# Performance work log

Hardware: AMD Instinct MI355X
Metric: run time of the kernel (lower is better)

Reference implementation:

```python
import jax, jax.numpy as jnp
import numpy as np

N, CM, CZ, COPM = 256, 384, 128, 32
HS, DHS = 8, 48   # row-attention heads / head dim (HS*DHS == CM)
HT, DHT = 4, 32   # triangle-attention heads / head dim


def _param_shapes():
    d = {'opm_ln': (2, CM), 'opm_lr_w': (2, CM, COPM), 'opm_lr_b': (2, COPM),
         'opm_out_w': (COPM, COPM, CZ), 'opm_out_b': (CZ,),
         'ra_ln': (2, CM), 'ra_pair_ln': (2, CZ), 'ra_feat_w': (CZ, HS),
         'ra_qkv_w': (3, CM, HS, DHS), 'ra_gate_w': (CM, HS, DHS), 'ra_gate_b': (HS, DHS),
         'ra_o_w': (HS, DHS, CM), 'ra_o_b': (CM,),
         'st_ln': (2, CM), 'st_w1': (CM, 4 * CM), 'st_b1': (4 * CM,), 'st_w2': (4 * CM, CM), 'st_b2': (CM,)}
    for p in ('tmo', 'tmi'):
        d.update({p + '_ln': (2, CZ), p + '_lr_w': (2, CZ, CZ), p + '_lr_b': (2, CZ),
                  p + '_gate_w': (2, CZ, CZ), p + '_gate_b': (2, CZ), p + '_cln': (2, CZ),
                  p + '_out_w': (CZ, CZ), p + '_out_b': (CZ,), p + '_og_w': (CZ, CZ), p + '_og_b': (CZ,)})
    for p in ('tas', 'tae'):
        d.update({p + '_ln': (2, CZ), p + '_feat_w': (CZ, HT), p + '_qkv_w': (3, CZ, HT, DHT),
                  p + '_gate_w': (CZ, HT, DHT), p + '_gate_b': (HT, DHT),
                  p + '_o_w': (HT, DHT, CZ), p + '_o_b': (CZ,)})
    d.update({'pt_ln': (2, CZ), 'pt_w1': (CZ, 4 * CZ), 'pt_b1': (4 * CZ,),
              'pt_w2': (4 * CZ, CZ), 'pt_b2': (CZ,)})
    return d

_PNAMES = list(_param_shapes().keys())


def setup_inputs():
    keys = iter(jax.random.split(jax.random.key(0), 64))
    inp = {'single_act': jax.random.normal(next(keys), (1, N, CM), jnp.float32),
           'pair_act': jax.random.normal(next(keys), (N, N, CZ), jnp.float32),
           'single_mask': jnp.ones((1, N), jnp.float32),
           'pair_mask': jnp.ones((N, N), jnp.float32)}
    for name, shp in _param_shapes().items():
        p = 0.1 * jax.random.normal(next(keys), shp, jnp.float32)
        if name.endswith('_ln') or name.endswith('_cln'):
            p = p.at[0].add(1.0)  # LayerNorm scale centered at 1
        inp[name] = p
    return inp


def _ln(x, p, eps=1e-5):
    mu = jnp.mean(x, -1, keepdims=True)
    var = jnp.var(x, -1, keepdims=True)
    return (x - mu) * jax.lax.rsqrt(var + eps) * p[0] + p[1]


def _attn(q_data, m_data, bias, nb, qkv_w, gw, gb, ow, ob):
    # AlphaFold gated attention with nonbatched pair bias.
    dh = qkv_w.shape[-1]
    q = jnp.einsum('bqa,ahc->bqhc', q_data, qkv_w[0]) * (dh ** -0.5)
    k = jnp.einsum('bka,ahc->bkhc', m_data, qkv_w[1])
    v = jnp.einsum('bka,ahc->bkhc', m_data, qkv_w[2])
    logits = jnp.einsum('bqhc,bkhc->bhqk', q, k) + bias + nb[None]
    w = jax.nn.softmax(logits, axis=-1)
    wa = jnp.einsum('bhqk,bkhc->bqhc', w, v)
    wa = wa * jax.nn.sigmoid(jnp.einsum('bqc,chv->bqhv', q_data, gw) + gb)
    return jnp.einsum('bqhc,hco->bqo', wa, ow) + ob


def _opm(single, mask1, ln_p, lr_w, lr_b, out_w, out_b):
    # Outer-stack(product)-mean: single [S=1,N,CM] -> pair update [N,N,CZ]
    x = _ln(single, ln_p)
    m = mask1[..., None]
    left = m * (x @ lr_w[0] + lr_b[0])    # [1,N,COPM]
    right = m * (x @ lr_w[1] + lr_b[1])
    act = jnp.einsum('abc,ade->dceb', left, right)          # [N,COPM,COPM,N]
    act = jnp.einsum('dceb,cef->dbf', act, out_w) + out_b   # [N,N,CZ]
    norm = jnp.einsum('abc,adc->bdc', m, m)                 # [N,N,1]
    return act / (1e-3 + norm)


def _tri_mult(pair, mask2, ln_p, lr_w, lr_b, gw, gb, cln, out_w, out_b, og_w, og_b, outgoing):
    m = mask2[..., None]
    x = _ln(pair, ln_p)
    left = m * (x @ lr_w[0] + lr_b[0]) * jax.nn.sigmoid(x @ gw[0] + gb[0])
    right = m * (x @ lr_w[1] + lr_b[1]) * jax.nn.sigmoid(x @ gw[1] + gb[1])
    eq = 'ikc,jkc->ijc' if outgoing else 'kjc,kic->ijc'
    out = jnp.einsum(eq, left, right)
    out = _ln(out, cln) @ out_w + out_b
    out = out * jax.nn.sigmoid(x @ og_w + og_b)
    return pair + out


def _tri_attn(pair, mask2, ln_p, feat_w, qkv_w, gw, gb, ow, ob, per_column):
    pa = jnp.swapaxes(pair, 0, 1) if per_column else pair
    mk = jnp.swapaxes(mask2, 0, 1) if per_column else mask2
    x = _ln(pa, ln_p)
    bias = (1e9 * (mk - 1.0))[:, None, None, :]
    nb = jnp.einsum('qkc,ch->hqk', x, feat_w)
    out = _attn(x, x, bias, nb, qkv_w, gw, gb, ow, ob)
    if per_column:
        out = jnp.swapaxes(out, 0, 1)
    return pair + out


def _fwd(sa, pa, sm, pm, p):
    # 1) outer stack mean -> pair residual
    pa = pa + _opm(sa, sm, p['opm_ln'], p['opm_lr_w'], p['opm_lr_b'], p['opm_out_w'], p['opm_out_b'])
    # 2) row attention with pair bias
    x = _ln(sa, p['ra_ln'])
    bias = (1e9 * (sm - 1.0))[:, None, None, :]
    nb = jnp.einsum('qkc,ch->hqk', _ln(pa, p['ra_pair_ln']), p['ra_feat_w'])
    sa = sa + _attn(x, x, bias, nb, p['ra_qkv_w'], p['ra_gate_w'], p['ra_gate_b'], p['ra_o_w'], p['ra_o_b'])
    # 3) single transition
    x = _ln(sa, p['st_ln'])
    sa = sa + jax.nn.relu(x @ p['st_w1'] + p['st_b1']) @ p['st_w2'] + p['st_b2']
    # 4/5) triangle multiplications
    ko = ('ln', 'lr_w', 'lr_b', 'gate_w', 'gate_b', 'cln', 'out_w', 'out_b', 'og_w', 'og_b')
    pa = _tri_mult(pa, pm, *[p['tmo_' + k] for k in ko], outgoing=True)
    pa = _tri_mult(pa, pm, *[p['tmi_' + k] for k in ko], outgoing=False)
    # 6/7) triangle attentions
    ka = ('ln', 'feat_w', 'qkv_w', 'gate_w', 'gate_b', 'o_w', 'o_b')
    pa = _tri_attn(pa, pm, *[p['tas_' + k] for k in ka], per_column=False)
    pa = _tri_attn(pa, pm, *[p['tae_' + k] for k in ka], per_column=True)
    # 8) pair transition
    x = _ln(pa, p['pt_ln'])
    pa = pa + jax.nn.relu(x @ p['pt_w1'] + p['pt_b1']) @ p['pt_w2'] + p['pt_b2']
    return sa, pa


def reference(single_act, pair_act, single_mask, pair_mask,
              opm_ln, opm_lr_w, opm_lr_b, opm_out_w, opm_out_b,
              ra_ln, ra_pair_ln, ra_feat_w, ra_qkv_w, ra_gate_w, ra_gate_b, ra_o_w, ra_o_b,
              st_ln, st_w1, st_b1, st_w2, st_b2,
              tmo_ln, tmo_lr_w, tmo_lr_b, tmo_gate_w, tmo_gate_b, tmo_cln, tmo_out_w, tmo_out_b, tmo_og_w, tmo_og_b,
              tmi_ln, tmi_lr_w, tmi_lr_b, tmi_gate_w, tmi_gate_b, tmi_cln, tmi_out_w, tmi_out_b, tmi_og_w, tmi_og_b,
              tas_ln, tas_feat_w, tas_qkv_w, tas_gate_w, tas_gate_b, tas_o_w, tas_o_b,
              tae_ln, tae_feat_w, tae_qkv_w, tae_gate_w, tae_gate_b, tae_o_w, tae_o_b,
              pt_ln, pt_w1, pt_b1, pt_w2, pt_b2):
    args = dict(locals())
    p = {k: args[k] for k in _PNAMES}
    return _fwd(single_act, pair_act, single_mask, pair_mask, p)
```

## Files before the change

### kernel.cpp

```cpp
#include <hip/hip_runtime.h>
#include <math.h>

typedef long long i64;
#define NN_ 65536L

typedef __attribute__((ext_vector_type(8))) short bf16x8;
typedef __attribute__((ext_vector_type(4))) float f32x4;

__device__ inline unsigned short f2bf(float f){
  unsigned int u = __float_as_uint(f);
  return (unsigned short)((u + 0x7FFFu + ((u>>16)&1u)) >> 16);
}

__global__ __launch_bounds__(256) void copy_k(float* __restrict__ d, const float* __restrict__ s, long n){
  long i = (long)blockIdx.x*blockDim.x + threadIdx.x;
  if (i < n) d[i] = s[i];
}

__global__ __launch_bounds__(256) void chw2hwc_k(const float* __restrict__ in, float* __restrict__ out){
  __shared__ float t[32][33];
  int r0 = blockIdx.x*32, c0 = blockIdx.y*32;
  int tx = threadIdx.x & 31, ty = threadIdx.x >> 5;
  for (int i = ty; i < 32; i += 8) t[i][tx] = in[(i64)(c0+i)*NN_ + r0 + tx];
  __syncthreads();
  for (int i = ty; i < 32; i += 8) out[(i64)(r0+i)*128 + c0 + tx] = t[tx][i];
}

__global__ __launch_bounds__(256) void tr_mask_k(const float* __restrict__ in, const float* __restrict__ mask,
                                                 float* __restrict__ out){
  __shared__ float t[32][33];
  int r0 = blockIdx.x*32, c0 = blockIdx.y*32;
  int tx = threadIdx.x & 31, ty = threadIdx.x >> 5;
  for (int i = ty; i < 32; i += 8) t[i][tx] = in[(i64)(r0+i)*128 + c0 + tx];
  __syncthreads();
  for (int i = ty; i < 32; i += 8) out[(i64)(c0+i)*NN_ + r0 + tx] = t[tx][i] * mask[r0+tx];
}

__global__ __launch_bounds__(256) void feat4_k(const float* __restrict__ X, const float* __restrict__ W,
                                               float* __restrict__ out){
  __shared__ float4 w_s[128];
  int q = blockIdx.x, k = threadIdx.x;
  if (k < 128) w_s[k] = *(const float4*)(W + k*4);
  __syncthreads();
  const float* x = X + ((i64)q*256 + k)*128;
  float a0=0.f, a1=0.f, a2=0.f, a3=0.f;
  #pragma unroll
  for (int c=0;c<128;c+=4){
    float4 v = *(const float4*)(x+c);
    float4 w0 = w_s[c], w1 = w_s[c+1], w2 = w_s[c+2], w3 = w_s[c+3];
    a0 = fmaf(v.x,w0.x,a0); a1 = fmaf(v.x,w0.y,a1); a2 = fmaf(v.x,w0.z,a2); a3 = fmaf(v.x,w0.w,a3);
    a0 = fmaf(v.y,w1.x,a0); a1 = fmaf(v.y,w1.y,a1); a2 = fmaf(v.y,w1.z,a2); a3 = fmaf(v.y,w1.w,a3);
    a0 = fmaf(v.z,w2.x,a0); a1 = fmaf(v.z,w2.y,a1); a2 = fmaf(v.z,w2.z,a2); a3 = fmaf(v.z,w2.w,a3);
    a0 = fmaf(v.w,w3.x,a0); a1 = fmaf(v.w,w3.y,a1); a2 = fmaf(v.w,w3.z,a2); a3 = fmaf(v.w,w3.w,a3);
  }
  i64 o = (i64)q*256 + k;
  out[o] = a0; out[65536+o] = a1; out[131072+o] = a2; out[196608+o] = a3;
}

__global__ __launch_bounds__(256) void feat8_k(const float* __restrict__ X, const float* __restrict__ W,
                                               float* __restrict__ out){
  __shared__ float w_s[128][8];
  int q = blockIdx.x, k = threadIdx.x;
  for (int i = k; i < 1024; i += 256) ((float*)w_s)[i] = W[i];
  __syncthreads();
  const float* x = X + ((i64)q*256 + k)*128;
  float acc[8] = {};
  #pragma unroll
  for (int c=0;c<128;c+=4){
    float4 v = *(const float4*)(x+c);
    #pragma unroll
    for (int h=0;h<8;h++){
      acc[h] = fmaf(v.x, w_s[c  ][h], acc[h]);
      acc[h] = fmaf(v.y, w_s[c+1][h], acc[h]);
      acc[h] = fmaf(v.z, w_s[c+2][h], acc[h]);
      acc[h] = fmaf(v.w, w_s[c+3][h], acc[h]);
    }
  }
  float* o = out + ((i64)q*256 + k)*8;
  *(float4*)o     = make_float4(acc[0],acc[1],acc[2],acc[3]);
  *(float4*)(o+4) = make_float4(acc[4],acc[5],acc[6],acc[7]);
}

__global__ __launch_bounds__(128) void ln_k(const float* __restrict__ in, float* __restrict__ out,
                                            const float* __restrict__ w, int C){
  i64 row = blockIdx.x;
  const float* x = in + row*C;
  float* y = out + row*C;
  int tid = threadIdx.x;
  float s=0.f, s2=0.f;
  for (int c=tid;c<C;c+=128){ float v = x[c]; s += v; s2 += v*v; }
  __shared__ float rs[128], rq[128];
  rs[tid]=s; rq[tid]=s2; __syncthreads();
  for (int off=64;off>0;off>>=1){ if (tid<off){ rs[tid]+=rs[tid+off]; rq[tid]+=rq[tid+off]; } __syncthreads(); }
  float mu = rs[0]/C;
  float var = rq[0]/C - mu*mu;
  float inv = rsqrtf(var + 1e-5f);
  for (int c=tid;c<C;c+=128) y[c] = (x[c]-mu)*inv*w[c] + w[C+c];
}

__global__ __launch_bounds__(256) void ln128_k(const float* __restrict__ in, float* __restrict__ out,
                                               const float* __restrict__ w, int T){
  int wv = threadIdx.x >> 6, lane = threadIdx.x & 63;
  i64 row = (i64)blockIdx.x*4 + wv;
  i64 rr = T ? (i64)((((int)row & 255) << 8) | ((int)row >> 8)) : row;
  float2 v = *(const float2*)(in + rr*128 + lane*2);
  float s = v.x + v.y, s2 = v.x*v.x + v.y*v.y;
  #pragma unroll
  for (int off=32; off; off>>=1){ s += __shfl_down(s, off); s2 += __shfl_down(s2, off); }
  s = __shfl(s, 0); s2 = __shfl(s2, 0);
  float mu = s*(1.f/128.f);
  float var = s2*(1.f/128.f) - mu*mu;
  float inv = rsqrtf(var + 1e-5f);
  float2 wl = *(const float2*)(w + lane*2);
  float2 wb = *(const float2*)(w + 128 + lane*2);
  float2 y; y.x = (v.x-mu)*inv*wl.x + wb.x; y.y = (v.y-mu)*inv*wl.y + wb.y;
  *(float2*)(out + row*128 + lane*2) = y;
}

template<bool TA, bool TB>
__global__ __launch_bounds__(256) void mgemm_k(
    const float* __restrict__ A, int lda, i64 sA,
    const float* __restrict__ B, int ldb, i64 sB,
    float* __restrict__ C, int ldc, i64 sC,
    int M, int N, int K,
    const float* __restrict__ bias, float scale, int act,
    const float* __restrict__ rowmul, int combine, const float* __restrict__ aux)
{
  A += (i64)blockIdx.z * sA;
  B += (i64)blockIdx.z * sB;
  C += (i64)blockIdx.z * sC;
  int m0 = blockIdx.x * 128, n0 = blockIdx.y * 128;
  int tid = threadIdx.x;
  int wave = tid >> 6, lane = tid & 63;
  int quad = lane >> 4, mr = lane & 15;
  int wm = (wave >> 1) * 64, wn = (wave & 1) * 64;
  __shared__ unsigned short As[128][40];
  __shared__ unsigned short Bs[128][40];
  f32x4 acc[4][4];
  #pragma unroll
  for (int i=0;i<4;i++)
    #pragma unroll
    for (int j=0;j<4;j++) acc[i][j] = (f32x4){0.f,0.f,0.f,0.f};

  for (int k0 = 0; k0 < K; k0 += 32){
    if (!TA){
      #pragma unroll
      for (int it=0; it<4; it++){
        int lin = tid + it*256;
        int r = lin >> 3, c4 = (lin & 7) * 4;
        float4 g = *(const float4*)&A[(i64)(m0+r)*lda + k0 + c4];
        As[r][c4]   = f2bf(g.x); As[r][c4+1] = f2bf(g.y);
        As[r][c4+2] = f2bf(g.z); As[r][c4+3] = f2bf(g.w);
      }
    } else {
      #pragma unroll
      for (int it=0; it<4; it++){
        int lin = tid + it*256;
        int m = lin & 127, kg = (lin >> 7) * 4;
        float v0 = A[(i64)(k0+kg  )*lda + m0 + m];
        float v1 = A[(i64)(k0+kg+1)*lda + m0 + m];
        float v2 = A[(i64)(k0+kg+2)*lda + m0 + m];
        float v3 = A[(i64)(k0+kg+3)*lda + m0 + m];
        As[m][kg] = f2bf(v0); As[m][kg+1] = f2bf(v1);
        As[m][kg+2] = f2bf(v2); As[m][kg+3] = f2bf(v3);
      }
    }
    if (!TB){
      #pragma unroll
      for (int it=0; it<4; it++){
        int lin = tid + it*256;
        int n = lin & 127, kg = (lin >> 7) * 4;
        float v0 = B[(i64)(k0+kg  )*ldb + n0 + n];
        float v1 = B[(i64)(k0+kg+1)*ldb + n0 + n];
        float v2 = B[(i64)(k0+kg+2)*ldb + n0 + n];
        float v3 = B[(i64)(k0+kg+3)*ldb + n0 + n];
        Bs[n][kg] = f2bf(v0); Bs[n][kg+1] = f2bf(v1);
        Bs[n][kg+2] = f2bf(v2); Bs[n][kg+3] = f2bf(v3);
      }
    } else {
      #pragma unroll
      for (int it=0; it<4; it++){
        int lin = tid + it*256;
        int r = lin >> 3, c4 = (lin & 7) * 4;
        float4 g = *(const float4*)&B[(i64)(n0+r)*ldb + k0 + c4];
        Bs[r][c4]   = f2bf(g.x); Bs[r][c4+1] = f2bf(g.y);
        Bs[r][c4+2] = f2bf(g.z); Bs[r][c4+3] = f2bf(g.w);
      }
    }
    __syncthreads();
    bf16x8 af[4], bfr[4];
    #pragma unroll
    for (int i=0;i<4;i++) af[i]  = *(const bf16x8*)&As[wm + i*16 + mr][quad*8];
    #pragma unroll
    for (int j=0;j<4;j++) bfr[j] = *(const bf16x8*)&Bs[wn + j*16 + mr][quad*8];
    #pragma unroll
    for (int i=0;i<4;i++)
      #pragma unroll
      for (int j=0;j<4;j++)
        acc[i][j] = __builtin_amdgcn_mfma_f32_16x16x32_bf16(af[i], bfr[j], acc[i][j], 0, 0, 0);
    __syncthreads();
  }
  #pragma unroll
  for (int i=0;i<4;i++){
    #pragma unroll
    for (int r=0;r<4;r++){
      int m = m0 + wm + i*16 + quad*4 + r;
      float rm = rowmul ? rowmul[m] : 1.f;
      i64 mrow = (combine == 4) ? (i64)(((m & 255) << 8) | (m >> 8)) : (i64)m;
      #pragma unroll
      for (int j=0;j<4;j++){
        int n = n0 + wn + j*16 + mr;
        float v = acc[i][j][r] * scale;
        if (bias) v += bias[n];
        if (act == 1) v = fmaxf(v, 0.f);
        else if (act == 2) v = 1.f/(1.f + __expf(-v));
        v *= rm;
        i64 idx = mrow*ldc + n;
        if (combine == 0) C[idx] = v;
        else if (combine == 1 || combine == 4) C[idx] += v;
        else if (combine == 2) C[idx] *= v;
        else C[idx] += aux[(i64)m*ldc + n] * v;
      }
    }
  }
}

template<bool TA, bool TB>
__global__ __launch_bounds__(256) void mgemm64_k(
    const float* __restrict__ A, int lda, i64 sA,
    const float* __restrict__ B, int ldb, i64 sB,
    float* __restrict__ C, int ldc, i64 sC,
    int M, int N, int K,
    const float* __restrict__ bias, float scale, int act,
    const float* __restrict__ rowmul, int combine, const float* __restrict__ aux)
{
  A += (i64)blockIdx.z * sA;
  B += (i64)blockIdx.z * sB;
  C += (i64)blockIdx.z * sC;
  int m0 = blockIdx.x * 64, n0 = blockIdx.y * 64;
  int tid = threadIdx.x;
  int wave = tid >> 6, lane = tid & 63;
  int quad = lane >> 4, mr = lane & 15;
  int wm = (wave >> 1) * 32, wn = (wave & 1) * 32;
  __shared__ unsigned short As[64][40];
  __shared__ unsigned short Bs[64][40];
  f32x4 acc[2][2];
  #pragma unroll
  for (int i=0;i<2;i++)
    #pragma unroll
    for (int j=0;j<2;j++) acc[i][j] = (f32x4){0.f,0.f,0.f,0.f};

  for (int k0 = 0; k0 < K; k0 += 32){
    if (!TA){
      #pragma unroll
      for (int it=0; it<2; it++){
        int lin = tid + it*256;
        int r = lin >> 3, c4 = (lin & 7) * 4;
        float4 g = *(const float4*)&A[(i64)(m0+r)*lda + k0 + c4];
        As[r][c4]   = f2bf(g.x); As[r][c4+1] = f2bf(g.y);
        As[r][c4+2] = f2bf(g.z); As[r][c4+3] = f2bf(g.w);
      }
    } else {
      #pragma unroll
      for (int it=0; it<2; it++){
        int lin = tid + it*256;
        int m = lin & 63, kg = (lin >> 6) * 4;
        float v0 = A[(i64)(k0+kg  )*lda + m0 + m];
        float v1 = A[(i64)(k0+kg+1)*lda + m0 + m];
        float v2 = A[(i64)(k0+kg+2)*lda + m0 + m];
        float v3 = A[(i64)(k0+kg+3)*lda + m0 + m];
        As[m][kg] = f2bf(v0); As[m][kg+1] = f2bf(v1);
        As[m][kg+2] = f2bf(v2); As[m][kg+3] = f2bf(v3);
      }
    }
    if (!TB){
      #pragma unroll
      for (int it=0; it<2; it++){
        int lin = tid + it*256;
        int n = lin & 63, kg = (lin >> 6) * 4;
        float v0 = B[(i64)(k0+kg  )*ldb + n0 + n];
        float v1 = B[(i64)(k0+kg+1)*ldb + n0 + n];
        float v2 = B[(i64)(k0+kg+2)*ldb + n0 + n];
        float v3 = B[(i64)(k0+kg+3)*ldb + n0 + n];
        Bs[n][kg] = f2bf(v0); Bs[n][kg+1] = f2bf(v1);
        Bs[n][kg+2] = f2bf(v2); Bs[n][kg+3] = f2bf(v3);
      }
    } else {
      #pragma unroll
      for (int it=0; it<2; it++){
        int lin = tid + it*256;
        int r = lin >> 3, c4 = (lin & 7) * 4;
        float4 g = *(const float4*)&B[(i64)(n0+r)*ldb + k0 + c4];
        Bs[r][c4]   = f2bf(g.x); Bs[r][c4+1] = f2bf(g.y);
        Bs[r][c4+2] = f2bf(g.z); Bs[r][c4+3] = f2bf(g.w);
      }
    }
    __syncthreads();
    bf16x8 af[2], bfr[2];
    #pragma unroll
    for (int i=0;i<2;i++) af[i]  = *(const bf16x8*)&As[wm + i*16 + mr][quad*8];
    #pragma unroll
    for (int j=0;j<2;j++) bfr[j] = *(const bf16x8*)&Bs[wn + j*16 + mr][quad*8];
    #pragma unroll
    for (int i=0;i<2;i++)
      #pragma unroll
      for (int j=0;j<2;j++)
        acc[i][j] = __builtin_amdgcn_mfma_f32_16x16x32_bf16(af[i], bfr[j], acc[i][j], 0, 0, 0);
    __syncthreads();
  }
  #pragma unroll
  for (int i=0;i<2;i++){
    #pragma unroll
    for (int r=0;r<4;r++){
      int m = m0 + wm + i*16 + quad*4 + r;
      float rm = rowmul ? rowmul[m] : 1.f;
      i64 mrow = (combine == 4) ? (i64)(((m & 255) << 8) | (m >> 8)) : (i64)m;
      #pragma unroll
      for (int j=0;j<2;j++){
        int n = n0 + wn + j*16 + mr;
        float v = acc[i][j][r] * scale;
        if (bias) v += bias[n];
        if (act == 1) v = fmaxf(v, 0.f);
        else if (act == 2) v = 1.f/(1.f + __expf(-v));
        v *= rm;
        i64 idx = mrow*ldc + n;
        if (combine == 0) C[idx] = v;
        else if (combine == 1 || combine == 4) C[idx] += v;
        else if (combine == 2) C[idx] *= v;
        else C[idx] += aux[(i64)m*ldc + n] * v;
      }
    }
  }
}

__global__ __launch_bounds__(256) void qkvb_k(
    const float* __restrict__ A, const float* __restrict__ B,
    unsigned short* __restrict__ C, float scale)
{
  int m0 = blockIdx.x * 64, n0 = blockIdx.y * 64;
  int tid = threadIdx.x;
  int wave = tid >> 6, lane = tid & 63;
  int quad = lane >> 4, mr = lane & 15;
  int wm = (wave >> 1) * 32, wn = (wave & 1) * 32;
  __shared__ unsigned short As[64][40];
  __shared__ unsigned short Bs[64][40];
  f32x4 acc[2][2];
  #pragma unroll
  for (int i=0;i<2;i++)
    #pragma unroll
    for (int j=0;j<2;j++) acc[i][j] = (f32x4){0.f,0.f,0.f,0.f};

  for (int k0 = 0; k0 < 128; k0 += 32){
    #pragma unroll
    for (int it=0; it<2; it++){
      int lin = tid + it*256;
      int r = lin >> 3, c4 = (lin & 7) * 4;
      float4 g = *(const float4*)&A[(i64)(m0+r)*128 + k0 + c4];
      As[r][c4]   = f2bf(g.x); As[r][c4+1] = f2bf(g.y);
      As[r][c4+2] = f2bf(g.z); As[r][c4+3] = f2bf(g.w);
    }
    #pragma unroll
    for (int it=0; it<2; it++){
      int lin = tid + it*256;
      int n = lin & 63, kg = (lin >> 6) * 4;
      float v0 = B[(i64)(k0+kg  )*128 + n0 + n];
      float v1 = B[(i64)(k0+kg+1)*128 + n0 + n];
      float v2 = B[(i64)(k0+kg+2)*128 + n0 + n];
      float v3 = B[(i64)(k0+kg+3)*128 + n0 + n];
      Bs[n][kg] = f2bf(v0); Bs[n][kg+1] = f2bf(v1);
      Bs[n][kg+2] = f2bf(v2); Bs[n][kg+3] = f2bf(v3);
    }
    __syncthreads();
    bf16x8 af[2], bfr[2];
    #pragma unroll
    for (int i=0;i<2;i++) af[i]  = *(const bf16x8*)&As[wm + i*16 + mr][quad*8];
    #pragma unroll
    for (int j=0;j<2;j++) bfr[j] = *(const bf16x8*)&Bs[wn + j*16 + mr][quad*8];
    #pragma unroll
    for (int i=0;i<2;i++)
      #pragma unroll
      for (int j=0;j<2;j++)
        acc[i][j] = __builtin_amdgcn_mfma_f32_16x16x32_bf16(af[i], bfr[j], acc[i][j], 0, 0, 0);
    __syncthreads();
  }
  #pragma unroll
  for (int i=0;i<2;i++){
    #pragma unroll
    for (int r=0;r<4;r++){
      int m = m0 + wm + i*16 + quad*4 + r;
      #pragma unroll
      for (int j=0;j<2;j++){
        int n = n0 + wn + j*16 + mr;
        C[(i64)m*128 + n] = f2bf(acc[i][j][r] * scale);
      }
    }
  }
}

__global__ __launch_bounds__(256) void mlrgate_k(
    const float* __restrict__ X,
    const float* __restrict__ Wl, const float* __restrict__ bl,
    const float* __restrict__ Wg, const float* __restrict__ bg,
    float* __restrict__ Out)
{
  int m0 = blockIdx.x * 64, n0 = blockIdx.y * 64;
  int tid = threadIdx.x;
  int wave = tid >> 6, lane = tid & 63;
  int quad = lane >> 4, mr = lane & 15;
  int wm = (wave >> 1) * 32, wn = (wave & 1) * 32;
  __shared__ unsigned short As[64][40], B1s[64][40], B2s[64][40];
  f32x4 acc1[2][2], acc2[2][2];
  #pragma unroll
  for (int i=0;i<2;i++)
    #pragma unroll
    for (int j=0;j<2;j++){ acc1[i][j] = (f32x4){0,0,0,0}; acc2[i][j] = (f32x4){0,0,0,0}; }

  for (int k0 = 0; k0 < 128; k0 += 32){
    #pragma unroll
    for (int it=0; it<2; it++){
      int lin = tid + it*256;
      int r = lin >> 3, c4 = (lin & 7) * 4;
      float4 g = *(const float4*)&X[(i64)(m0+r)*128 + k0 + c4];
      As[r][c4]   = f2bf(g.x); As[r][c4+1] = f2bf(g.y);
      As[r][c4+2] = f2bf(g.z); As[r][c4+3] = f2bf(g.w);
    }
    #pragma unroll
    for (int it=0; it<2; it++){
      int lin = tid + it*256;
      int n = lin & 63, kg = (lin >> 6) * 4;
      float a0 = Wl[(i64)(k0+kg  )*128 + n0 + n];
      float a1 = Wl[(i64)(k0+kg+1)*128 + n0 + n];
      float a2 = Wl[(i64)(k0+kg+2)*128 + n0 + n];
      float a3 = Wl[(i64)(k0+kg+3)*128 + n0 + n];
      B1s[n][kg] = f2bf(a0); B1s[n][kg+1] = f2bf(a1);
      B1s[n][kg+2] = f2bf(a2); B1s[n][kg+3] = f2bf(a3);
      float g0 = Wg[(i64)(k0+kg  )*128 + n0 + n];
      float g1 = Wg[(i64)(k0+kg+1)*128 + n0 + n];
      float g2 = Wg[(i64)(k0+kg+2)*128 + n0 + n];
      float g3 = Wg[(i64)(k0+kg+3)*128 + n0 + n];
      B2s[n][kg] = f2bf(g0); B2s[n][kg+1] = f2bf(g1);
      B2s[n][kg+2] = f2bf(g2); B2s[n][kg+3] = f2bf(g3);
    }
    __syncthreads();
    bf16x8 af[2], b1f[2], b2f[2];
    #pragma unroll
    for (int i=0;i<2;i++) af[i]  = *(const bf16x8*)&As[wm + i*16 + mr][quad*8];
    #pragma unroll
    for (int j=0;j<2;j++){
      b1f[j] = *(const bf16x8*)&B1s[wn + j*16 + mr][quad*8];
      b2f[j] = *(const bf16x8*)&B2s[wn + j*16 + mr][quad*8];
    }
    #pragma unroll
    for (int i=0;i<2;i++)
      #pragma unroll
      for (int j=0;j<2;j++){
        acc1[i][j] = __builtin_amdgcn_mfma_f32_16x16x32_bf16(af[i], b1f[j], acc1[i][j], 0, 0, 0);
        acc2[i][j] = __builtin_amdgcn_mfma_f32_16x16x32_bf16(af[i], b2f[j], acc2[i][j], 0, 0, 0);
      }
    __syncthreads();
  }
  #pragma unroll
  for (int i=0;i<2;i++){
    #pragma unroll
    for (int r=0;r<4;r++){
      int m = m0 + wm + i*16 + quad*4 + r;
      #pragma unroll
      for (int j=0;j<2;j++){
        int n = wn + j*16 + mr;
        float lv = acc1[i][j][r] + bl[n0 + n];
        float gv = acc2[i][j][r] + bg[n0 + n];
        Out[(i64)m*128 + n0 + n] = lv * (1.f/(1.f + __expf(-gv)));
      }
    }
  }
}

__global__ __launch_bounds__(256) void ptw1_k(
    const float* __restrict__ X, const float* __restrict__ W1,
    const float* __restrict__ b1, unsigned short* __restrict__ H)
{
  int m0 = blockIdx.x * 128, n0 = blockIdx.y * 128;
  int tid = threadIdx.x;
  int wave = tid >> 6, lane = tid & 63;
  int quad = lane >> 4, mr = lane & 15;
  int wm = (wave >> 1) * 64, wn = (wave & 1) * 64;
  __shared__ unsigned short As[128][40];
  __shared__ unsigned short Bs[128][40];
  f32x4 acc[4][4];
  #pragma unroll
  for (int i=0;i<4;i++)
    #pragma unroll
    for (int j=0;j<4;j++) acc[i][j] = (f32x4){0.f,0.f,0.f,0.f};

  for (int k0 = 0; k0 < 128; k0 += 32){
    #pragma unroll
    for (int it=0; it<4; it++){
      int lin = tid + it*256;
      int r = lin >> 3, c4 = (lin & 7) * 4;
      float4 g = *(const float4*)&X[(i64)(m0+r)*128 + k0 + c4];
      As[r][c4]   = f2bf(g.x); As[r][c4+1] = f2bf(g.y);
      As[r][c4+2] = f2bf(g.z); As[r][c4+3] = f2bf(g.w);
    }
    #pragma unroll
    for (int it=0; it<4; it++){
      int lin = tid + it*256;
      int n = lin & 127, kg = (lin >> 7) * 4;
      float v0 = W1[(i64)(k0+kg  )*512 + n0 + n];
      float v1 = W1[(i64)(k0+kg+1)*512 + n0 + n];
      float v2 = W1[(i64)(k0+kg+2)*512 + n0 + n];
      float v3 = W1[(i64)(k0+kg+3)*512 + n0 + n];
      Bs[n][kg] = f2bf(v0); Bs[n][kg+1] = f2bf(v1);
      Bs[n][kg+2] = f2bf(v2); Bs[n][kg+3] = f2bf(v3);
    }
    __syncthreads();
    bf16x8 af[4], bfr[4];
    #pragma unroll
    for (int i=0;i<4;i++) af[i]  = *(const bf16x8*)&As[wm + i*16 + mr][quad*8];
    #pragma unroll
    for (int j=0;j<4;j++) bfr[j] = *(const bf16x8*)&Bs[wn + j*16 + mr][quad*8];
    #pragma unroll
    for (int i=0;i<4;i++)
      #pragma unroll
      for (int j=0;j<4;j++)
        acc[i][j] = __builtin_amdgcn_mfma_f32_16x16x32_bf16(af[i], bfr[j], acc[i][j], 0, 0, 0);
    __syncthreads();
  }
  #pragma unroll
  for (int i=0;i<4;i++){
    #pragma unroll
    for (int r=0;r<4;r++){
      int m = m0 + wm + i*16 + quad*4 + r;
      #pragma unroll
      for (int j=0;j<4;j++){
        int n = n0 + wn + j*16 + mr;
        float v = fmaxf(acc[i][j][r] + b1[n], 0.f);
        H[(i64)m*512 + n] = f2bf(v);
      }
    }
  }
}

__global__ __launch_bounds__(256) void ptw2_k(
    const unsigned short* __restrict__ H, const float* __restrict__ W2,
    const float* __restrict__ b2, float* __restrict__ pa)
{
  int m0 = blockIdx.x * 64, n0 = blockIdx.y * 64;
  int tid = threadIdx.x;
  int wave = tid >> 6, lane = tid & 63;
  int quad = lane >> 4, mr = lane & 15;
  int wm = (wave >> 1) * 32, wn = (wave & 1) * 32;
  __shared__ unsigned short As[64][40];
  __shared__ unsigned short Bs[64][40];
  f32x4 acc[2][2];
  #pragma unroll
  for (int i=0;i<2;i++)
    #pragma unroll
    for (int j=0;j<2;j++) acc[i][j] = (f32x4){0.f,0.f,0.f,0.f};

  for (int k0 = 0; k0 < 512; k0 += 32){
    #pragma unroll
    for (int it=0; it<2; it++){
      int lin = tid + it*256;
      int r = lin >> 3, c4 = (lin & 7) * 4;
      *(uint2*)&As[r][c4] = *(const uint2*)&H[(i64)(m0+r)*512 + k0 + c4];
    }
    #pragma unroll
    for (int it=0; it<2; it++){
      int lin = tid + it*256;
      int n = lin & 63, kg = (lin >> 6) * 4;
      float v0 = W2[(i64)(k0+kg  )*128 + n0 + n];
      float v1 = W2[(i64)(k0+kg+1)*128 + n0 + n];
      float v2 = W2[(i64)(k0+kg+2)*128 + n0 + n];
      float v3 = W2[(i64)(k0+kg+3)*128 + n0 + n];
      Bs[n][kg] = f2bf(v0); Bs[n][kg+1] = f2bf(v1);
      Bs[n][kg+2] = f2bf(v2); Bs[n][kg+3] = f2bf(v3);
    }
    __syncthreads();
    bf16x8 af[2], bfr[2];
    #pragma unroll
    for (int i=0;i<2;i++) af[i]  = *(const bf16x8*)&As[wm + i*16 + mr][quad*8];
    #pragma unroll
    for (int j=0;j<2;j++) bfr[j] = *(const bf16x8*)&Bs[wn + j*16 + mr][quad*8];
    #pragma unroll
    for (int i=0;i<2;i++)
      #pragma unroll
      for (int j=0;j<2;j++)
        acc[i][j] = __builtin_amdgcn_mfma_f32_16x16x32_bf16(af[i], bfr[j], acc[i][j], 0, 0, 0);
    __syncthreads();
  }
  #pragma unroll
  for (int i=0;i<2;i++){
    #pragma unroll
    for (int r=0;r<4;r++){
      int m = m0 + wm + i*16 + quad*4 + r;
      #pragma unroll
      for (int j=0;j<2;j++){
        int n = n0 + wn + j*16 + mr;
        pa[(i64)m*128 + n] += acc[i][j][r] + b2[n];
      }
    }
  }
}

template<bool TA, bool TB>
__global__ __launch_bounds__(256) void gemm_k(
    const float* __restrict__ A, int lda, i64 sA,
    const float* __restrict__ B, int ldb, i64 sB,
    float* __restrict__ C, int ldc, i64 sC,
    int M, int N, int K,
    const float* __restrict__ bias, float scale, int act,
    const float* __restrict__ rowmul, int combine)
{
  A += (i64)blockIdx.z * sA;
  B += (i64)blockIdx.z * sB;
  C += (i64)blockIdx.z * sC;
  int m0 = blockIdx.x * 64, n0 = blockIdx.y * 64;
  int tid = threadIdx.x, tx = tid & 15, ty = tid >> 4;
  __shared__ float As[16][68], Bs[16][68];
  float acc[4][4] = {};
  for (int k0 = 0; k0 < K; k0 += 16){
    if (TA){
      for (int l = tid; l < 1024; l += 256){
        int kk = l >> 6, mi = l & 63; int m = m0 + mi;
        As[kk][mi] = (m < M) ? A[(i64)(k0+kk)*lda + m] : 0.f;
      }
    } else {
      for (int l = tid; l < 1024; l += 256){
        int mi = l >> 4, kk = l & 15; int m = m0 + mi;
        As[kk][mi] = (m < M) ? A[(i64)m*lda + k0 + kk] : 0.f;
      }
    }
    if (TB){
      for (int l = tid; l < 1024; l += 256){
        int ni = l >> 4, kk = l & 15; int n = n0 + ni;
        Bs[kk][ni] = (n < N) ? B[(i64)n*ldb + k0 + kk] : 0.f;
      }
    } else {
      for (int l = tid; l < 1024; l += 256){
        int kk = l >> 6, ni = l & 63; int n = n0 + ni;
        Bs[kk][ni] = (n < N) ? B[(i64)(k0+kk)*ldb + n] : 0.f;
      }
    }
    __syncthreads();
    #pragma unroll
    for (int kk = 0; kk < 16; ++kk){
      float4 av4 = *(const float4*)&As[kk][ty*4];
      float4 bv4 = *(const float4*)&Bs[kk][tx*4];
      float av[4] = {av4.x, av4.y, av4.z, av4.w};
      float bv[4] = {bv4.x, bv4.y, bv4.z, bv4.w};
      #pragma unroll
      for (int i=0;i<4;i++)
        #pragma unroll
        for (int j=0;j<4;j++) acc[i][j] = fmaf(av[i], bv[j], acc[i][j]);
    }
    __syncthreads();
  }
  #pragma unroll
  for (int i=0;i<4;i++){
    int m = m0 + ty*4 + i;
    if (m >= M) continue;
    float rm = rowmul ? rowmul[m] : 1.f;
    #pragma unroll
    for (int j=0;j<4;j++){
      int n = n0 + tx*4 + j;
      if (n >= N) continue;
      float v = acc[i][j] * scale;
      if (bias) v += bias[n];
      if (act == 1) v = fmaxf(v, 0.f);
      else if (act == 2) v = 1.f/(1.f + expf(-v));
      v *= rm;
      i64 idx = (i64)m*ldc + n;
      if (combine == 0) C[idx] = v;
      else if (combine == 1) C[idx] += v;
      else C[idx] *= v;
    }
  }
}

__global__ __launch_bounds__(256) void gemm_part_k(
    const float* __restrict__ A, int lda,
    const float* __restrict__ B, int ldb,
    float* __restrict__ Cp, int M, int N, int K, int chunk)
{
  int m0 = blockIdx.x*16, n0 = blockIdx.y*64, z = blockIdx.z;
  int kb = z*chunk, ke = min(K, kb+chunk);
  int tid = threadIdx.x;
  int mi = tid >> 4, ni4 = (tid & 15)*4;
  __shared__ float As[16][17], Bs[16][68];
  float acc[4] = {0.f,0.f,0.f,0.f};
  for (int k0 = kb; k0 < ke; k0 += 16){
    { int r = tid>>4, c = tid&15; int m = m0+r;
      As[c][r] = (m < M) ? A[(i64)m*lda + k0 + c] : 0.f; }
    for (int l = tid; l < 1024; l += 256){
      int kk = l>>6, nn = l&63; int n = n0+nn;
      Bs[kk][nn] = (n < N) ? B[(i64)(k0+kk)*ldb + n] : 0.f;
    }
    __syncthreads();
    #pragma unroll
    for (int kk=0;kk<16;kk++){
      float a = As[kk][mi];
      float4 b = *(const float4*)&Bs[kk][ni4];
      acc[0]=fmaf(a,b.x,acc[0]); acc[1]=fmaf(a,b.y,acc[1]);
      acc[2]=fmaf(a,b.z,acc[2]); acc[3]=fmaf(a,b.w,acc[3]);
    }
    __syncthreads();
  }
  int m = m0+mi, n = n0+ni4;
  if (m < M && n < N) *(float4*)&Cp[((i64)z*M + m)*N + n] = *(float4*)acc;
}

__global__ __launch_bounds__(256) void gemm_reduce_k(
    const float* __restrict__ Cp, float* __restrict__ C, int ldc,
    int M, int N, int S,
    const float* __restrict__ bias, float scale, int act,
    const float* __restrict__ rowmul, int combine)
{
  i64 idx = (i64)blockIdx.x*256 + threadIdx.x;
  if (idx >= (i64)M*N) return;
  int m = (int)(idx / N), n = (int)(idx % N);
  float s = 0.f;
  for (int z=0; z<S; z++) s += Cp[(i64)z*M*N + idx];
  float v = s*scale;
  if (bias) v += bias[n];
  if (act == 1) v = fmaxf(v, 0.f);
  else if (act == 2) v = 1.f/(1.f + expf(-v));
  if (rowmul) v *= rowmul[m];
  i64 o = (i64)m*ldc + n;
  if (combine == 0) C[o] = v;
  else if (combine == 1) C[o] += v;
  else C[o] *= v;
}

__global__ __launch_bounds__(128) void opm_wd_k(const float* __restrict__ right, const float* __restrict__ W,
                                                float* __restrict__ Wd){
  int d = blockIdx.x, c = blockIdx.y, f = threadIdx.x;
  float acc = 0.f;
  #pragma unroll
  for (int e=0;e<32;e++) acc = fmaf(right[d*32+e], W[((i64)c*32+e)*128 + f], acc);
  Wd[((i64)d*32+c)*128 + f] = acc;
}

__global__ __launch_bounds__(128) void opm_final_k(const float* __restrict__ left, const float* __restrict__ Wd,
                                                   const float* __restrict__ ob, const float* __restrict__ sm,
                                                   const float* __restrict__ pair_act, float* __restrict__ pa){
  int d = blockIdx.x, b0 = blockIdx.y*16, f = threadIdx.x;
  __shared__ float wd_s[32][128];
  __shared__ float l_s[16][32];
  for (int c=0;c<32;c++) wd_s[c][f] = Wd[((i64)d*32+c)*128 + f];
  for (int l = f; l < 512; l += 128){ int bi=l>>5, c=l&31; l_s[bi][c] = left[(b0+bi)*32 + c]; }
  __syncthreads();
  float md = sm[d], obf = ob[f];
  for (int bi=0;bi<16;bi++){
    float acc = 0.f;
    #pragma unroll
    for (int c=0;c<32;c++) acc = fmaf(l_s[bi][c], wd_s[c][f], acc);
    int b = b0+bi;
    i64 idx = ((i64)d*256 + b)*128 + f;
    pa[idx] = pair_act[idx] + (acc + obf) / (1e-3f + md*sm[b]);
  }
}

__global__ __launch_bounds__(256) void ra_attn_k(const float* __restrict__ q, const float* __restrict__ k,
                                                 const float* __restrict__ v, const float* __restrict__ nb,
                                                 const float* __restrict__ sm, float* __restrict__ wa){
  int qi = blockIdx.x, h = blockIdx.y, tid = threadIdx.x;
  __shared__ float qv[48];
  __shared__ float p[256];
  __shared__ float red[256];
  if (tid < 48) qv[tid] = q[(i64)qi*384 + h*48 + tid];
  __syncthreads();
  float acc = 0.f;
  const float* kr = k + (i64)tid*384 + h*48;
  #pragma unroll
  for (int c=0;c<48;c++) acc = fmaf(qv[c], kr[c], acc);
  acc += 1e9f*(sm[tid]-1.f) + nb[((i64)qi*256 + tid)*8 + h];
  red[tid] = acc; __syncthreads();
  for (int off=128;off>0;off>>=1){ if (tid<off) red[tid] = fmaxf(red[tid], red[tid+off]); __syncthreads(); }
  float mx = red[0]; __syncthreads();
  float e = expf(acc - mx);
  red[tid] = e; __syncthreads();
  for (int off=128;off>0;off>>=1){ if (tid<off) red[tid] += red[tid+off]; __syncthreads(); }
  p[tid] = e / red[0];
  __syncthreads();
  if (tid < 48){
    float a = 0.f;
    for (int kk=0;kk<256;kk++) a = fmaf(p[kk], v[(i64)kk*384 + h*48 + tid], a);
    wa[(i64)qi*384 + h*48 + tid] = a;
  }
}

__global__ __launch_bounds__(256, 6) void ta_mfma_k(
    const unsigned short* __restrict__ q, const unsigned short* __restrict__ k,
    const unsigned short* __restrict__ v,
    const float* __restrict__ nbQ, const float* __restrict__ mask, int maskT,
    float* __restrict__ wa)
{
  int d = blockIdx.x;
  int xcd = d & 7, y = d >> 3;
  int b = xcd*32 + (y >> 4);
  int w = y & 15;
  int qblk = w & 3, h = w >> 2;
  int tid = threadIdx.x;
  int wave = tid >> 6, lane = tid & 63;
  int quad = lane >> 4, mr = lane & 15;
  const i64 base = ((i64)b*256)*128 + h*32;

  __shared__ __align__(16) unsigned short Ks[128][40];
  __shared__ __align__(16) unsigned short Vt[32][136];
  __shared__ __align__(16) float mask_s[256];
  __shared__ __align__(16) unsigned short Pl[4][16][40];

  mask_s[tid] = 1e9f * ((maskT ? mask[(i64)tid*256 + b] : mask[(i64)b*256 + tid]) - 1.f);

  int q0w = qblk*64 + wave*16;
  int qg = q0w + mr;
  const float* nbq = nbQ + (i64)h*65536 + (i64)qg*256;

  bf16x8 qf = *(const bf16x8*)(q + base + (i64)qg*128 + quad*8);

  f32x4 o0 = (f32x4){0,0,0,0}, o1 = (f32x4){0,0,0,0};
  float mm = -1e30f, ll = 0.f;

  for (int half = 0; half < 2; half++){
    __syncthreads();
    #pragma unroll
    for (int it=0; it<4; it++){
      int idx = it*256 + tid;
      int kl = idx >> 3, c4 = (idx & 7)*4;
      i64 roff = base + (i64)(half*128 + kl)*128 + c4;
      *(uint2*)&Ks[kl][c4] = *(const uint2*)(k + roff);
      uint2 gv = *(const uint2*)(v + roff);
      const unsigned short* pv = (const unsigned short*)&gv;
      Vt[c4  ][kl] = pv[0];
      Vt[c4+1][kl] = pv[1];
      Vt[c4+2][kl] = pv[2];
      Vt[c4+3][kl] = pv[3];
    }
    __syncthreads();

    #pragma unroll
    for (int it=0; it<4; it++){
      int kc = it*32;
      int kg = half*128 + kc;
      bf16x8 kf0 = *(const bf16x8*)&Ks[kc + mr][quad*8];
      bf16x8 kf1 = *(const bf16x8*)&Ks[kc + 16 + mr][quad*8];
      f32x4 s0 = __builtin_amdgcn_mfma_f32_16x16x32_bf16(kf0, qf, (f32x4){0,0,0,0}, 0, 0, 0);
      f32x4 s1 = __builtin_amdgcn_mfma_f32_16x16x32_bf16(kf1, qf, (f32x4){0,0,0,0}, 0, 0, 0);
      float4 nb0 = *(const float4*)(nbq + kg + quad*4);
      float4 nb1 = *(const float4*)(nbq + kg + 16 + quad*4);
      float4 mk0 = *(const float4*)&mask_s[kg + quad*4];
      float4 mk1 = *(const float4*)&mask_s[kg + 16 + quad*4];
      s0[0] += nb0.x + mk0.x; s0[1] += nb0.y + mk0.y; s0[2] += nb0.z + mk0.z; s0[3] += nb0.w + mk0.w;
      s1[0] += nb1.x + mk1.x; s1[1] += nb1.y + mk1.y; s1[2] += nb1.z + mk1.z; s1[3] += nb1.w + mk1.w;

      float tm = fmaxf(fmaxf(fmaxf(s0[0],s0[1]), fmaxf(s0[2],s0[3])),
                       fmaxf(fmaxf(s1[0],s1[1]), fmaxf(s1[2],s1[3])));
      tm = fmaxf(tm, __shfl_xor(tm, 16));
      tm = fmaxf(tm, __shfl_xor(tm, 32));
      float nm = fmaxf(mm, tm);
      float alpha = __expf(mm - nm);
      mm = nm;
      float e00 = __expf(s0[0]-nm), e01 = __expf(s0[1]-nm);
      float e02 = __expf(s0[2]-nm), e03 = __expf(s0[3]-nm);
      float e10 = __expf(s1[0]-nm), e11 = __expf(s1[1]-nm);
      float e12 = __expf(s1[2]-nm), e13 = __expf(s1[3]-nm);
      float ps = ((e00+e01) + (e02+e03)) + ((e10+e11) + (e12+e13));
      ps += __shfl_xor(ps, 16);
      ps += __shfl_xor(ps, 32);
      ll = ll*alpha + ps;
      o0 *= alpha; o1 *= alpha;
      unsigned int p0 = (unsigned int)f2bf(e00) | ((unsigned int)f2bf(e01)<<16);
      unsigned int p1 = (unsigned int)f2bf(e02) | ((unsigned int)f2bf(e03)<<16);
      unsigned int p2 = (unsigned int)f2bf(e10) | ((unsigned int)f2bf(e11)<<16);
      unsigned int p3 = (unsigned int)f2bf(e12) | ((unsigned int)f2bf(e13)<<16);
      *(uint2*)&Pl[wave][mr][quad*4]      = make_uint2(p0, p1);
      *(uint2*)&Pl[wave][mr][16 + quad*4] = make_uint2(p2, p3);
      bf16x8 pf  = *(const bf16x8*)&Pl[wave][mr][quad*8];
      bf16x8 vf0 = *(const bf16x8*)&Vt[mr     ][kc + quad*8];
      bf16x8 vf1 = *(const bf16x8*)&Vt[16 + mr][kc + quad*8];
      o0 = __builtin_amdgcn_mfma_f32_16x16x32_bf16(vf0, pf, o0, 0, 0, 0);
      o1 = __builtin_amdgcn_mfma_f32_16x16x32_bf16(vf1, pf, o1, 0, 0, 0);
    }
  }

  float inv = 1.f/ll;
  float* wp = wa + base + (i64)qg*128;
  *(float4*)(wp + quad*4)      = make_float4(o0[0]*inv, o0[1]*inv, o0[2]*inv, o0[3]*inv);
  *(float4*)(wp + 16 + quad*4) = make_float4(o1[0]*inv, o1[1]*inv, o1[2]*inv, o1[3]*inv);
}

static void gemm(hipStream_t st, bool TA, bool TB,
                 const float* A, int lda, i64 sA,
                 const float* B, int ldb, i64 sB,
                 float* C, int ldc, i64 sC,
                 int M, int N, int K, int batch,
                 const float* bias, float scale, int act,
                 const float* rowmul, int combine)
{
  dim3 g((M+63)/64, (N+63)/64, batch), bl(256);
  if (!TA && !TB)      gemm_k<false,false><<<g,bl,0,st>>>(A,lda,sA,B,ldb,sB,C,ldc,sC,M,N,K,bias,scale,act,rowmul,combine);
  else if (!TA &&  TB) gemm_k<false,true ><<<g,bl,0,st>>>(A,lda,sA,B,ldb,sB,C,ldc,sC,M,N,K,bias,scale,act,rowmul,combine);
  else                 gemm_k<true ,false><<<g,bl,0,st>>>(A,lda,sA,B,ldb,sB,C,ldc,sC,M,N,K,bias,scale,act,rowmul,combine);
}

static void mgemm(hipStream_t st, bool TA, bool TB,
                  const float* A, int lda, i64 sA,
                  const float* B, int ldb, i64 sB,
                  float* C, int ldc, i64 sC,
                  int M, int N, int K, int batch,
                  const float* bias, float scale, int act,
                  const float* rowmul, int combine, const float* aux = nullptr)
{
  dim3 bl(256);
  i64 nb128 = (i64)(M/128)*(N/128)*batch;
  if (nb128 < 1024 && (M % 64) == 0 && (N % 64) == 0){
    dim3 g(M/64, N/64, batch);
    if (!TA && !TB)      mgemm64_k<false,false><<<g,bl,0,st>>>(A,lda,sA,B,ldb,sB,C,ldc,sC,M,N,K,bias,scale,act,rowmul,combine,aux);
    else if (!TA &&  TB) mgemm64_k<false,true ><<<g,bl,0,st>>>(A,lda,sA,B,ldb,sB,C,ldc,sC,M,N,K,bias,scale,act,rowmul,combine,aux);
    else                 mgemm64_k<true ,false><<<g,bl,0,st>>>(A,lda,sA,B,ldb,sB,C,ldc,sC,M,N,K,bias,scale,act,rowmul,combine,aux);
    return;
  }
  dim3 g(M/128, N/128, batch);
  if (!TA && !TB)      mgemm_k<false,false><<<g,bl,0,st>>>(A,lda,sA,B,ldb,sB,C,ldc,sC,M,N,K,bias,scale,act,rowmul,combine,aux);
  else if (!TA &&  TB) mgemm_k<false,true ><<<g,bl,0,st>>>(A,lda,sA,B,ldb,sB,C,ldc,sC,M,N,K,bias,scale,act,rowmul,combine,aux);
  else                 mgemm_k<true ,false><<<g,bl,0,st>>>(A,lda,sA,B,ldb,sB,C,ldc,sC,M,N,K,bias,scale,act,rowmul,combine,aux);
}

static void gemm_thin(hipStream_t st,
                      const float* A, int lda, const float* B, int ldb,
                      float* C, int ldc, int M, int N, int K,
                      const float* bias, float scale, int act,
                      const float* rowmul, int combine, float* part)
{
  const int S = 8;
  int chunk = ((K/S + 15)/16)*16; if (chunk < 16) chunk = 16;
  dim3 g((M+15)/16, (N+63)/64, S);
  gemm_part_k<<<g,256,0,st>>>(A,lda,B,ldb,part,M,N,K,chunk);
  i64 t = (i64)M*N;
  gemm_reduce_k<<<(int)((t+255)/256),256,0,st>>>(part,C,ldc,M,N,S,bias,scale,act,rowmul,combine);
}

extern "C" void kernel_launch(void* const* d_in, const int* in_sizes, int n_in,
                              void* d_out, int out_size, void* d_ws, size_t ws_size,
                              hipStream_t stream)
{
  const float* IN[64];
  for (int i=0;i<n_in && i<64;i++) IN[i] = (const float*)d_in[i];

  const float* single_act = IN[0];
  const float* pair_act   = IN[1];
  const float* sm         = IN[2];
  const float* pm         = IN[3];
  const float* opm_ln     = IN[4];
  const float* opm_lr_w   = IN[5];
  const float* opm_lr_b   = IN[6];
  const float* opm_out_w  = IN[7];
  const float* opm_out_b  = IN[8];
  const float* ra_ln      = IN[9];
  const float* ra_pair_ln = IN[10];
  const float* ra_feat_w  = IN[11];
  const float* ra_qkv_w   = IN[12];
  const float* ra_gate_w  = IN[13];
  const float* ra_gate_b  = IN[14];
  const float* ra_o_w     = IN[15];
  const float* ra_o_b     = IN[16];
  const float* st_ln      = IN[17];
  const float* st_w1      = IN[18];
  const float* st_b1      = IN[19];
  const float* st_w2      = IN[20];
  const float* st_b2      = IN[21];
  const float* pt_ln      = IN[56];
  const float* pt_w1      = IN[57];
  const float* pt_b1      = IN[58];
  const float* pt_w2      = IN[59];
  const float* pt_b2      = IN[60];

  float* sa = (float*)d_out;
  float* pa = (float*)d_out + 98304;

  float* W  = (float*)d_ws;
  float* B0 = W;
  float* B1 = W + 8388608L;
  float* B2 = W + 16777216L;
  float* B3 = W + 25165824L;
  float* SMA = W + 33554432L;
  float* xs   = SMA;
  float* qb   = SMA +  98304;
  float* kb   = SMA + 196608;
  float* vb   = SMA + 294912;
  float* wab  = SMA + 393216;
  float* hst  = SMA + 491520;
  float* nbra = SMA + 884736;
  float* lbuf = SMA + 1409024;
  float* rbuf = SMA + 1417216;
  float* Wd   = SMA + 1425408;

  unsigned short* qb16 = (unsigned short*)B2;
  unsigned short* kb16 = (unsigned short*)B2 + 8388608L;
  unsigned short* vb16 = (unsigned short*)B3;

  copy_k<<<384, 256, 0, stream>>>(sa, single_act, 98304L);

  ln_k<<<256,128,0,stream>>>(single_act, xs, opm_ln, 384);
  gemm_thin(stream, xs,384, opm_lr_w,32,       lbuf,32, 256,32,384, opm_lr_b,    1.f,0, sm,0, B1);
  gemm_thin(stream, xs,384, opm_lr_w+12288,32, rbuf,32, 256,32,384, opm_lr_b+32, 1.f,0, sm,0, B1);
  opm_wd_k<<<dim3(256,32),128,0,stream>>>(rbuf, opm_out_w, Wd);
  opm_final_k<<<dim3(256,16),128,0,stream>>>(lbuf, Wd, opm_out_b, sm, pair_act, pa);

  ln_k<<<256,128,0,stream>>>(sa, xs, ra_ln, 384);
  ln128_k<<<16384,256,0,stream>>>(pa, B0, ra_pair_ln, 0);
  feat8_k<<<256,256,0,stream>>>(B0, ra_feat_w, nbra);
  const float qs_ra = 0.14433756729740643f;
  gemm_thin(stream, xs,384, ra_qkv_w,384,        qb,384, 256,384,384, nullptr,qs_ra,0,nullptr,0, B1);
  gemm_thin(stream, xs,384, ra_qkv_w+147456,384, kb,384, 256,384,384, nullptr,1.f,0,nullptr,0, B1);
  gemm_thin(stream, xs,384, ra_qkv_w+294912,384, vb,384, 256,384,384, nullptr,1.f,0,nullptr,0, B1);
  ra_attn_k<<<dim3(256,8),256,0,stream>>>(qb, kb, vb, nbra, sm, wab);
  gemm_thin(stream, xs,384,  ra_gate_w,384, wab,384, 256,384,384, ra_gate_b,1.f,2,nullptr,2, B1);
  gemm_thin(stream, wab,384, ra_o_w,384,    sa,384,  256,384,384, ra_o_b,   1.f,0,nullptr,1, B1);

  ln_k<<<256,128,0,stream>>>(sa, xs, st_ln, 384);
  gemm_thin(stream, xs,384,   st_w1,1536, hst,1536, 256,1536,384, st_b1,1.f,1,nullptr,0, B1);
  gemm_thin(stream, hst,1536, st_w2,384,  sa,384,   256,384,1536, st_b2,1.f,0,nullptr,1, B1);

  auto tri_mult = [&](int base, bool outgoing){
    const float* ln_w = IN[base+0];
    const float* lr_w = IN[base+1];
    const float* lr_b = IN[base+2];
    const float* gw   = IN[base+3];
    const float* gb   = IN[base+4];
    const float* cln  = IN[base+5];
    const float* ow   = IN[base+6];
    const float* ob   = IN[base+7];
    const float* ogw  = IN[base+8];
    const float* ogb  = IN[base+9];
    ln128_k<<<16384,256,0,stream>>>(pa, B0, ln_w, 0);
    mlrgate_k<<<dim3(1024,2),256,0,stream>>>(B0, lr_w, lr_b, gw, gb, B3);
    tr_mask_k<<<dim3(2048,4),256,0,stream>>>(B3, pm, B1);
    mlrgate_k<<<dim3(1024,2),256,0,stream>>>(B0, lr_w+16384, lr_b+128, gw+16384, gb+128, B3);
    tr_mask_k<<<dim3(2048,4),256,0,stream>>>(B3, pm, B2);
    if (outgoing)
      mgemm(stream,false,true, B1,256,65536, B2,256,65536, B3,256,65536, 256,256,256,128, nullptr,1.f,0,nullptr,0);
    else
      mgemm(stream,true,false, B2,256,65536, B1,256,65536, B3,256,65536, 256,256,256,128, nullptr,1.f,0,nullptr,0);
    chw2hwc_k<<<dim3(2048,4),256,0,stream>>>(B3, B1);
    ln128_k<<<16384,256,0,stream>>>(B1, B3, cln, 0);
    mgemm(stream,false,false, B3,128,0, ow,128,0,  B1,128,0, 65536,128,128,1, ob,  1.f,0,nullptr,0);
    mgemm(stream,false,false, B0,128,0, ogw,128,0, pa,128,0, 65536,128,128,1, ogb, 1.f,2,nullptr,3, B1);
  };
  tri_mult(22, true);
  tri_mult(32, false);

  auto tri_attn = [&](int base, bool percol){
    const float* ln_w   = IN[base+0];
    const float* feat_w = IN[base+1];
    const float* qkv_w  = IN[base+2];
    const float* gw     = IN[base+3];
    const float* gb     = IN[base+4];
    const float* ow     = IN[base+5];
    const float* ob     = IN[base+6];
    ln128_k<<<16384,256,0,stream>>>(pa, B0, ln_w, percol?1:0);
    feat4_k<<<256,256,0,stream>>>(B0, feat_w, nbra);
    const float qs = 0.17677669529663687f;
    qkvb_k<<<dim3(1024,2),256,0,stream>>>(B0, qkv_w,       qb16, qs);
    qkvb_k<<<dim3(1024,2),256,0,stream>>>(B0, qkv_w+16384, kb16, 1.f);
    qkvb_k<<<dim3(1024,2),256,0,stream>>>(B0, qkv_w+32768, vb16, 1.f);
    ta_mfma_k<<<dim3(4096),256,0,stream>>>(qb16, kb16, vb16, nbra, pm, percol?1:0, B1);
    mgemm(stream,false,false, B0,128,0, gw,128,0, B1,128,0, 65536,128,128,1, gb,1.f,2,nullptr,2);
    mgemm(stream,false,false, B1,128,0, ow,128,0, pa,128,0, 65536,128,128,1, ob,1.f,0,nullptr, percol?4:1);
  };
  tri_attn(42, false);
  tri_attn(49, true);

  ln128_k<<<16384,256,0,stream>>>(pa, B0, pt_ln, 0);
  ptw1_k<<<dim3(512,4),256,0,stream>>>(B0, pt_w1, pt_b1, (unsigned short*)B1);
  ptw2_k<<<dim3(1024,2),256,0,stream>>>((const unsigned short*)B1, pt_w2, pt_b2, pa);
}
```

Baseline: 1.329 ms.

## Fuse transpose and mask into gated projection; shrink triangle-attention K/V tiles

The gated linear projection in triangle multiplication now stages its output tile in shared memory, reused from the GEMM operand buffers. It then writes the result transposed and masked directly to channel-major layout. This removes the separate transpose-mask kernel and one full read/write round trip of a 32 MB intermediate per projection. Separately, triangle attention processes keys in four 64-row chunks instead of two 128-row chunks, reducing LDS so the occupancy hint can rise from 6 to 8 blocks, at the cost of more synchronisation points.

```diff
diff --git a/kernel.cpp b/kernel.cpp
--- a/kernel.cpp
+++ b/kernel.cpp
@@ -24,16 +24,6 @@
   for (int i = ty; i < 32; i += 8) t[i][tx] = in[(i64)(c0+i)*NN_ + r0 + tx];
   __syncthreads();
   for (int i = ty; i < 32; i += 8) out[(i64)(r0+i)*128 + c0 + tx] = t[tx][i];
-}
-
-__global__ __launch_bounds__(256) void tr_mask_k(const float* __restrict__ in, const float* __restrict__ mask,
-                                                 float* __restrict__ out){
-  __shared__ float t[32][33];
-  int r0 = blockIdx.x*32, c0 = blockIdx.y*32;
-  int tx = threadIdx.x & 31, ty = threadIdx.x >> 5;
-  for (int i = ty; i < 32; i += 8) t[i][tx] = in[(i64)(r0+i)*128 + c0 + tx];
-  __syncthreads();
-  for (int i = ty; i < 32; i += 8) out[(i64)(c0+i)*NN_ + r0 + tx] = t[tx][i] * mask[r0+tx];
 }
 
 __global__ __launch_bounds__(256) void feat4_k(const float* __restrict__ X, const float* __restrict__ W,
@@ -397,18 +387,22 @@
   }
 }
 
-__global__ __launch_bounds__(256) void mlrgate_k(
+__global__ __launch_bounds__(256) void mlrgateT_k(
     const float* __restrict__ X,
     const float* __restrict__ Wl, const float* __restrict__ bl,
     const float* __restrict__ Wg, const float* __restrict__ bg,
-    float* __restrict__ Out)
+    const float* __restrict__ mask, float* __restrict__ Out)
 {
   int m0 = blockIdx.x * 64, n0 = blockIdx.y * 64;
   int tid = threadIdx.x;
   int wave = tid >> 6, lane = tid & 63;
   int quad = lane >> 4, mr = lane & 15;
   int wm = (wave >> 1) * 32, wn = (wave & 1) * 32;
-  __shared__ unsigned short As[64][40], B1s[64][40], B2s[64][40];
+  __shared__ __align__(16) char smem[16640];
+  unsigned short (*As)[40]  = (unsigned short(*)[40])(smem);
+  unsigned short (*B1s)[40] = (unsigned short(*)[40])(smem + 5120);
+  unsigned short (*B2s)[40] = (unsigned short(*)[40])(smem + 10240);
+  float (*T)[65] = (float(*)[65])(smem);
   f32x4 acc1[2][2], acc2[2][2];
   #pragma unroll
   for (int i=0;i<2;i++)
@@ -463,15 +457,28 @@
   for (int i=0;i<2;i++){
     #pragma unroll
     for (int r=0;r<4;r++){
-      int m = m0 + wm + i*16 + quad*4 + r;
+      int ml = wm + i*16 + quad*4 + r;
       #pragma unroll
       for (int j=0;j<2;j++){
-        int n = wn + j*16 + mr;
-        float lv = acc1[i][j][r] + bl[n0 + n];
-        float gv = acc2[i][j][r] + bg[n0 + n];
-        Out[(i64)m*128 + n0 + n] = lv * (1.f/(1.f + __expf(-gv)));
-      }
-    }
+        int nl = wn + j*16 + mr;
+        float lv = acc1[i][j][r] + bl[n0 + nl];
+        float gv = acc2[i][j][r] + bg[n0 + nl];
+        T[nl][ml] = lv * (1.f/(1.f + __expf(-gv)));
+      }
+    }
+  }
+  __syncthreads();
+  int n = tid >> 2, ms = (tid & 3) * 16;
+  const float* mk = mask + m0 + ms;
+  float* op = Out + (i64)(n0 + n)*NN_ + m0 + ms;
+  #pragma unroll
+  for (int e=0; e<16; e+=4){
+    float4 t4;
+    t4.x = T[n][ms+e]   * mk[e];
+    t4.y = T[n][ms+e+1] * mk[e+1];
+    t4.z = T[n][ms+e+2] * mk[e+2];
+    t4.w = T[n][ms+e+3] * mk[e+3];
+    *(float4*)(op + e) = t4;
   }
 }
 
@@ -789,7 +796,7 @@
   }
 }
 
-__global__ __launch_bounds__(256, 6) void ta_mfma_k(
+__global__ __launch_bounds__(256, 8) void ta_mfma_k(
     const unsigned short* __restrict__ q, const unsigned short* __restrict__ k,
     const unsigned short* __restrict__ v,
     const float* __restrict__ nbQ, const float* __restrict__ mask, int maskT,
@@ -805,8 +812,8 @@
   int quad = lane >> 4, mr = lane & 15;
   const i64 base = ((i64)b*256)*128 + h*32;
 
-  __shared__ __align__(16) unsigned short Ks[128][40];
-  __shared__ __align__(16) unsigned short Vt[32][136];
+  __shared__ __align__(16) unsigned short Ks[64][40];
+  __shared__ __align__(16) unsigned short Vt[32][72];
   __shared__ __align__(16) float mask_s[256];
   __shared__ __align__(16) unsigned short Pl[4][16][40];
 
@@ -821,13 +828,13 @@
   f32x4 o0 = (f32x4){0,0,0,0}, o1 = (f32x4){0,0,0,0};
   float mm = -1e30f, ll = 0.f;
 
-  for (int half = 0; half < 2; half++){
-    __syncthreads();
-    #pragma unroll
-    for (int it=0; it<4; it++){
+  for (int qt = 0; qt < 4; qt++){
+    __syncthreads();
+    #pragma unroll
+    for (int it=0; it<2; it++){
       int idx = it*256 + tid;
       int kl = idx >> 3, c4 = (idx & 7)*4;
-      i64 roff = base + (i64)(half*128 + kl)*128 + c4;
+      i64 roff = base + (i64)(qt*64 + kl)*128 + c4;
       *(uint2*)&Ks[kl][c4] = *(const uint2*)(k + roff);
       uint2 gv = *(const uint2*)(v + roff);
       const unsigned short* pv = (const unsigned short*)&gv;
@@ -839,9 +846,9 @@
     __syncthreads();
 
     #pragma unroll
-    for (int it=0; it<4; it++){
+    for (int it=0; it<2; it++){
       int kc = it*32;
-      int kg = half*128 + kc;
+      int kg = qt*64 + kc;
       bf16x8 kf0 = *(const bf16x8*)&Ks[kc + mr][quad*8];
       bf16x8 kf1 = *(const bf16x8*)&Ks[kc + 16 + mr][quad*8];
       f32x4 s0 = __builtin_amdgcn_mfma_f32_16x16x32_bf16(kf0, qf, (f32x4){0,0,0,0}, 0, 0, 0);
@@ -1034,10 +1041,8 @@
     const float* ogw  = IN[base+8];
     const float* ogb  = IN[base+9];
     ln128_k<<<16384,256,0,stream>>>(pa, B0, ln_w, 0);
-    mlrgate_k<<<dim3(1024,2),256,0,stream>>>(B0, lr_w, lr_b, gw, gb, B3);
-    tr_mask_k<<<dim3(2048,4),256,0,stream>>>(B3, pm, B1);
-    mlrgate_k<<<dim3(1024,2),256,0,stream>>>(B0, lr_w+16384, lr_b+128, gw+16384, gb+128, B3);
-    tr_mask_k<<<dim3(2048,4),256,0,stream>>>(B3, pm, B2);
+    mlrgateT_k<<<dim3(1024,2),256,0,stream>>>(B0, lr_w, lr_b, gw, gb, pm, B1);
+    mlrgateT_k<<<dim3(1024,2),256,0,stream>>>(B0, lr_w+16384, lr_b+128, gw+16384, gb+128, pm, B2);
     if (outgoing)
       mgemm(stream,false,true, B1,256,65536, B2,256,65536, B3,256,65536, 256,256,256,128, nullptr,1.f,0,nullptr,0);
     else
```

After: 1.272 ms. 1.04x faster.
